# Performance work log

Hardware: AMD Instinct MI355X
Metric: run time of the kernel (lower is better)

Reference implementation:

```python
import jax, jax.numpy as jnp
import numpy as np

B, TE, TD, H = 4, 1024, 512, 128


def setup_inputs() -> dict:
    key = jax.random.key(0)
    k1, k2, k3, k4, k5 = jax.random.split(key, 5)
    return {
        "encoder_out": jax.random.normal(k1, (B, TE, H), dtype=jnp.float32),
        "decoder_out": jax.random.normal(k2, (B, TD, H), dtype=jnp.float32),
        "W_a": jax.random.normal(k3, (H, H), dtype=jnp.float32) * 0.05,
        "U_a": jax.random.normal(k4, (H, H), dtype=jnp.float32) * 0.05,
        "V_a": jax.random.normal(k5, (H, 1), dtype=jnp.float32) * 0.05,
    }


def reference(encoder_out, decoder_out, W_a, U_a, V_a):
    # Bahdanau additive attention, vectorized over all decoder steps at once.
    # (The original K.rnn loop has no true recurrence; steps are independent.)
    W_s = jnp.einsum('bth,hk->btk', encoder_out, W_a)   # [B, Te, H]
    U_h = jnp.einsum('bdh,hk->bdk', decoder_out, U_a)   # [B, Td, H]
    # energies: v^T tanh(W s_t + U h_d) -> [B, Td, Te]
    tanh_arg = jnp.tanh(W_s[:, None, :, :] + U_h[:, :, None, :])  # [B, Td, Te, H]
    e = jnp.einsum('bdth,ho->bdt', tanh_arg, V_a)
    e = jax.nn.softmax(e, axis=-1)                      # attention weights [B, Td, Te]
    # context vectors: weighted sum over encoder positions -> [B, Td, H]
    c = jnp.einsum('bdt,bth->bdh', e, encoder_out)
    return (c, e)
```

## Files before the change

kernel.cpp:

```cpp
#include <hip/hip_runtime.h>

#define BB    4
#define TE    1024
#define TD    512
#define HH    128
#define DTILE 4
#define TTILE 64
#define ESTR  (TE + 8)
#define LOG2E 1.4426950408889634f

typedef float f32x2 __attribute__((ext_vector_type(2)));

__device__ __forceinline__ f32x2 pk_fma(f32x2 a, f32x2 b, f32x2 c) {
    return __builtin_elementwise_fma(a, b, c);
}

__device__ __forceinline__ float tanh_eval(float x) {
    float e = __builtin_amdgcn_exp2f(2.0f * LOG2E * x);
    return 1.0f - 2.0f * __builtin_amdgcn_rcpf(e + 1.0f);
}

__global__ __launch_bounds__(512, 2) void proj_gemm(
    const float* __restrict__ enc, const float* __restrict__ dec,
    const float* __restrict__ Wa,  const float* __restrict__ Ua,
    float* __restrict__ out)
{
    __shared__ float Ws[HH * HH];
    __shared__ float Xs[16 * HH];

    const int tid = threadIdx.x;
    const int r0  = blockIdx.x * 16;

    const float* X; const float* W; int rX0;
    if (r0 < BB * TE) { X = enc; W = Wa; rX0 = r0; }
    else              { X = dec; W = Ua; rX0 = r0 - BB * TE; }

    #pragma unroll
    for (int i = 0; i < 8; ++i)
        *(float4*)&Ws[i * 2048 + tid * 4] =
            *(const float4*)&W[i * 2048 + tid * 4];

    {
        const int r = tid >> 5, c = tid & 31;
        *(float4*)&Xs[r * HH + c * 4] =
            *(const float4*)&X[(size_t)(rX0 + r) * HH + c * 4];
    }
    __syncthreads();

    const int rr = tid >> 5;
    const int c4 = tid & 31;

    f32x2 aL0 = {0.f, 0.f}, aH0 = {0.f, 0.f};
    f32x2 aL1 = {0.f, 0.f}, aH1 = {0.f, 0.f};

    const float* wc   = &Ws[c4 * 4];
    const float* xrow = &Xs[rr * HH];

    #pragma unroll 4
    for (int k = 0; k < HH; k += 4) {
        float4 w0 = *(const float4*)&wc[(k + 0) * HH];
        float4 w1 = *(const float4*)&wc[(k + 1) * HH];
        float4 w2 = *(const float4*)&wc[(k + 2) * HH];
        float4 w3 = *(const float4*)&wc[(k + 3) * HH];
        float4 xv = *(const float4*)&xrow[k];

        aL0 = pk_fma((f32x2){xv.x, xv.x}, (f32x2){w0.x, w0.y}, aL0);
        aH0 = pk_fma((f32x2){xv.x, xv.x}, (f32x2){w0.z, w0.w}, aH0);
        aL1 = pk_fma((f32x2){xv.y, xv.y}, (f32x2){w1.x, w1.y}, aL1);
        aH1 = pk_fma((f32x2){xv.y, xv.y}, (f32x2){w1.z, w1.w}, aH1);
        aL0 = pk_fma((f32x2){xv.z, xv.z}, (f32x2){w2.x, w2.y}, aL0);
        aH0 = pk_fma((f32x2){xv.z, xv.z}, (f32x2){w2.z, w2.w}, aH0);
        aL1 = pk_fma((f32x2){xv.w, xv.w}, (f32x2){w3.x, w3.y}, aL1);
        aH1 = pk_fma((f32x2){xv.w, xv.w}, (f32x2){w3.z, w3.w}, aH1);
    }

    f32x2 aL = aL0 + aL1;
    f32x2 aH = aH0 + aH1;

    float4 o;
    o.x = tanh_eval(aL.x); o.y = tanh_eval(aL.y);
    o.z = tanh_eval(aH.x); o.w = tanh_eval(aH.y);
    *(float4*)&out[(size_t)(r0 + rr) * HH + c4 * 4] = o;
}

__global__ __launch_bounds__(512, 4) void attn_fused(
    const float* __restrict__ enc,
    const float* __restrict__ ta,
    const float* __restrict__ tb,
    const float* __restrict__ Va,
    float* __restrict__ c_out,
    float* __restrict__ e_out)
{
    __shared__ float e_s[DTILE * ESTR];
    __shared__ float p_s[DTILE * TE];
    __shared__ float c_red[8 * DTILE * HH];

    const int tid = threadIdx.x;
    const int l   = tid & 63;
    const int w   = tid >> 6;
    const int b   = blockIdx.x >> 7;
    const int d0  = (blockIdx.x & 127) * DTILE;

    const int h4 = l & 31, tsub = l >> 5;
    const float* enc_w = enc + ((size_t)b * TE + w * 8) * HH;
    float4 X0[4], X1[4];
    #pragma unroll
    for (int k = 0; k < 4; ++k)
        X0[k] = *(const float4*)&enc_w[(size_t)(tsub * 4 + k) * HH + h4 * 4];

    {
        const int g  = l >> 3;
        const int hl = l & 7;
        const int dl = g & 3;
        const int rh = g >> 2;

        f32x2 Bl[4], Bh[4], Pl[4], Ph[4], Vl[4], Vh[4];
        #pragma unroll
        for (int j = 0; j < 4; ++j) {
            float4 vv = *(const float4*)&Va[(j * 8 + hl) * 4];
            float4 bb = *(const float4*)&tb[((size_t)b * TD + d0 + dl) * HH + (j * 8 + hl) * 4];
            Vl[j] = (f32x2){vv.x, vv.y};  Vh[j] = (f32x2){vv.z, vv.w};
            Bl[j] = (f32x2){bb.x, bb.y};  Bh[j] = (f32x2){bb.z, bb.w};
            Pl[j] = Vl[j] * Bl[j];        Ph[j] = Vh[j] * Bh[j];
        }

        const float* ta_b = ta + (size_t)b * TE * HH;

        auto rowOf = [&](int i) {
            return ((i >> 2) << 6) + w * 8 + ((i & 3) << 1) + rh;
        };

        float4 A0[4], A1[4];
        auto loadA = [&](int i, float4 (&A)[4]) {
            const float* base = ta_b + (size_t)rowOf(i) * HH;
            #pragma unroll
            for (int j = 0; j < 4; ++j)
                A[j] = *(const float4*)&base[(j * 8 + hl) * 4];
        };

        auto p1c = [&](int i, float4 (&A)[4]) {
            const f32x2 one2 = {1.0f, 1.0f};
            f32x2 n2[8], d2[8];
            #pragma unroll
            for (int j = 0; j < 4; ++j) {
                f32x2 Al = (f32x2){A[j].x, A[j].y};
                f32x2 Ah = (f32x2){A[j].z, A[j].w};
                n2[2 * j]     = pk_fma(Vl[j], Al, Pl[j]);
                n2[2 * j + 1] = pk_fma(Vh[j], Ah, Ph[j]);
                d2[2 * j]     = pk_fma(Al, Bl[j], one2);
                d2[2 * j + 1] = pk_fma(Ah, Bh[j], one2);
            }
            #pragma unroll
            for (int s = 4; s >= 1; s >>= 1) {
                #pragma unroll
                for (int k = 0; k < s; ++k) {
                    n2[k] = pk_fma(n2[2 * k], d2[2 * k + 1], n2[2 * k + 1] * d2[2 * k]);
                    d2[k] = d2[2 * k] * d2[2 * k + 1];
                }
            }
            float num = n2[0].x * d2[0].y + n2[0].y * d2[0].x;
            float den = d2[0].x * d2[0].y;
            float e = num * __builtin_amdgcn_rcpf(den);
            e += __shfl_xor(e, 1);
            e += __shfl_xor(e, 2);
            e += __shfl_xor(e, 4);
            if (hl == 0) e_s[dl * ESTR + rowOf(i)] = e;
        };

        loadA(0, A0);
        #pragma unroll 1
        for (int i = 0; i < 62; i += 2) {
            loadA(i + 1, A1);
            p1c(i, A0);
            loadA(i + 2, A0);
            p1c(i + 1, A1);
        }
        loadA(63, A1);
        p1c(62, A0);
        p1c(63, A1);
    }
    __syncthreads();

    {
        const int d2 = w & 3, hf = w >> 2;
        float ev[16];
        float m = -3.0e38f;
        #pragma unroll
        for (int i = 0; i < 16; ++i) {
            ev[i] = e_s[d2 * ESTR + i * 64 + l];
            m = fmaxf(m, ev[i]);
        }
        #pragma unroll
        for (int off = 32; off; off >>= 1) m = fmaxf(m, __shfl_xor(m, off));
        float s = 0.f;
        #pragma unroll
        for (int i = 0; i < 16; ++i) {
            ev[i] = __builtin_amdgcn_exp2f((ev[i] - m) * LOG2E);
            s += ev[i];
        }
        #pragma unroll
        for (int off = 32; off; off >>= 1) s += __shfl_xor(s, off);
        float inv = __builtin_amdgcn_rcpf(s);

        float* eo = e_out + ((size_t)b * TD + d0 + d2) * TE;
        #pragma unroll
        for (int i = 0; i < 8; ++i) {
            int ii = hf * 8 + i;
            float p = ev[ii] * inv;
            p_s[d2 * TE + ii * 64 + l] = p;
            eo[ii * 64 + l] = p;
        }
        __syncthreads();
    }

    f32x2 accL[DTILE], accH[DTILE];
    #pragma unroll
    for (int d = 0; d < DTILE; ++d) {
        accL[d] = (f32x2){0.f, 0.f};
        accH[d] = (f32x2){0.f, 0.f};
    }

    {
        auto loadX = [&](int tt, float4 (&X)[4]) {
            const float* base = enc_w + (size_t)tt * TTILE * HH;
            #pragma unroll
            for (int k = 0; k < 4; ++k)
                X[k] = *(const float4*)&base[(tsub * 4 + k) * HH + h4 * 4];
        };

        auto p3c = [&](int tt, float4 (&X)[4]) {
            float4 ep[DTILE];
            #pragma unroll
            for (int d = 0; d < DTILE; ++d)
                ep[d] = *(const float4*)&p_s[d * TE + tt * TTILE + w * 8 + tsub * 4];
            #pragma unroll
            for (int k = 0; k < 4; ++k) {
                f32x2 xL = (f32x2){X[k].x, X[k].y};
                f32x2 xH = (f32x2){X[k].z, X[k].w};
                #pragma unroll
                for (int d = 0; d < DTILE; ++d) {
                    float p = k == 0 ? ep[d].x : k == 1 ? ep[d].y
                            : k == 2 ? ep[d].z : ep[d].w;
                    f32x2 pv = (f32x2){p, p};
                    accL[d] = pk_fma(pv, xL, accL[d]);
                    accH[d] = pk_fma(pv, xH, accH[d]);
                }
            }
        };

        #pragma unroll 1
        for (int tt = 0; tt < 14; tt += 2) {
            loadX(tt + 1, X1);
            p3c(tt, X0);
            loadX(tt + 2, X0);
            p3c(tt + 1, X1);
        }
        loadX(15, X1);
        p3c(14, X0);
        p3c(15, X1);
    }

    float4 acc4[DTILE];
    #pragma unroll
    for (int d = 0; d < DTILE; ++d)
        acc4[d] = make_float4(accL[d].x, accL[d].y, accH[d].x, accH[d].y);
    #pragma unroll
    for (int d = 0; d < DTILE; ++d) {
        acc4[d].x += __shfl_xor(acc4[d].x, 32);
        acc4[d].y += __shfl_xor(acc4[d].y, 32);
        acc4[d].z += __shfl_xor(acc4[d].z, 32);
        acc4[d].w += __shfl_xor(acc4[d].w, 32);
    }
    if (tsub == 0) {
        #pragma unroll
        for (int d = 0; d < DTILE; ++d)
            *(float4*)&c_red[(w * DTILE + d) * HH + h4 * 4] = acc4[d];
    }
    __syncthreads();

    if (w < DTILE && l < 32) {
        float4 o = make_float4(0.f, 0.f, 0.f, 0.f);
        #pragma unroll
        for (int ww = 0; ww < 8; ++ww) {
            float4 p = *(const float4*)&c_red[(ww * DTILE + w) * HH + l * 4];
            o.x += p.x; o.y += p.y; o.z += p.z; o.w += p.w;
        }
        *(float4*)&c_out[((size_t)b * TD + d0 + w) * HH + l * 4] = o;
    }
}

extern "C" void kernel_launch(void* const* d_in, const int* in_sizes, int n_in,
                              void* d_out, int out_size, void* d_ws, size_t ws_size,
                              hipStream_t stream) {
    (void)in_sizes; (void)n_in; (void)out_size; (void)ws_size;

    const float* enc = (const float*)d_in[0];
    const float* dec = (const float*)d_in[1];
    const float* Wa  = (const float*)d_in[2];
    const float* Ua  = (const float*)d_in[3];
    const float* Va  = (const float*)d_in[4];

    float* c_out = (float*)d_out;
    float* e_out = (float*)d_out + BB * TD * HH;

    float* proj = (float*)d_ws;
    float* ta_p = proj;
    float* tb_p = proj + BB * TE * HH;

    proj_gemm<<<384, 512, 0, stream>>>(enc, dec, Wa, Ua, proj);
    attn_fused<<<(BB * TD) / DTILE, 512, 0, stream>>>(enc, ta_p, tb_p, Va, c_out, e_out);
}
```

Measured before the change: 121.4 us.

## Split fused attention kernel into separate energy/softmax and context kernels

Splits the single fused attention kernel into two launches. The first computes energies and softmax and writes the weights to the output. The second reloads those weights from global memory into shared memory and computes the context vectors. The aim is to cut shared-memory and register pressure per kernel so more blocks fit per CU, and to let each phase schedule independently. In exchange it adds a launch and a global round trip of the attention weights.

```diff
diff --git a/kernel.cpp b/kernel.cpp
--- a/kernel.cpp
+++ b/kernel.cpp
@@ -83,30 +83,19 @@
     *(float4*)&out[(size_t)(r0 + rr) * HH + c4 * 4] = o;
 }
 
-__global__ __launch_bounds__(512, 4) void attn_fused(
-    const float* __restrict__ enc,
+__global__ __launch_bounds__(512, 4) void attn_energy(
     const float* __restrict__ ta,
     const float* __restrict__ tb,
     const float* __restrict__ Va,
-    float* __restrict__ c_out,
     float* __restrict__ e_out)
 {
     __shared__ float e_s[DTILE * ESTR];
-    __shared__ float p_s[DTILE * TE];
-    __shared__ float c_red[8 * DTILE * HH];
 
     const int tid = threadIdx.x;
     const int l   = tid & 63;
     const int w   = tid >> 6;
     const int b   = blockIdx.x >> 7;
     const int d0  = (blockIdx.x & 127) * DTILE;
-
-    const int h4 = l & 31, tsub = l >> 5;
-    const float* enc_w = enc + ((size_t)b * TE + w * 8) * HH;
-    float4 X0[4], X1[4];
-    #pragma unroll
-    for (int k = 0; k < 4; ++k)
-        X0[k] = *(const float4*)&enc_w[(size_t)(tsub * 4 + k) * HH + h4 * 4];
 
     {
         const int g  = l >> 3;
@@ -206,12 +195,42 @@
         #pragma unroll
         for (int i = 0; i < 8; ++i) {
             int ii = hf * 8 + i;
-            float p = ev[ii] * inv;
-            p_s[d2 * TE + ii * 64 + l] = p;
-            eo[ii * 64 + l] = p;
-        }
-        __syncthreads();
-    }
+            eo[ii * 64 + l] = ev[ii] * inv;
+        }
+    }
+}
+
+__global__ __launch_bounds__(512, 4) void attn_ctx(
+    const float* __restrict__ enc,
+    const float* __restrict__ e_out,
+    float* __restrict__ c_out)
+{
+    __shared__ float p_s[DTILE * TE];
+    __shared__ float c_red[8 * DTILE * HH];
+
+    const int tid = threadIdx.x;
+    const int l   = tid & 63;
+    const int w   = tid >> 6;
+    const int b   = blockIdx.x >> 7;
+    const int d0  = (blockIdx.x & 127) * DTILE;
+
+    const int h4 = l & 31, tsub = l >> 5;
+    const float* enc_w = enc + ((size_t)b * TE + w * 8) * HH;
+
+    float4 X0[4], X1[4];
+    #pragma unroll
+    for (int k = 0; k < 4; ++k)
+        X0[k] = *(const float4*)&enc_w[(size_t)(tsub * 4 + k) * HH + h4 * 4];
+
+    {
+        const float* po = e_out + ((size_t)b * TD + d0) * TE;
+        #pragma unroll
+        for (int i = 0; i < 2; ++i) {
+            int idx = tid + i * 512;
+            *(float4*)&p_s[idx * 4] = *(const float4*)&po[idx * 4];
+        }
+    }
+    __syncthreads();
 
     f32x2 accL[DTILE], accH[DTILE];
     #pragma unroll
@@ -307,6 +326,7 @@
     float* ta_p = proj;
     float* tb_p = proj + BB * TE * HH;
 
-    proj_gemm<<<384, 512, 0, stream>>>(enc, dec, Wa, Ua, proj);
-    attn_fused<<<(BB * TD) / DTILE, 512, 0, stream>>>(enc, ta_p, tb_p, Va, c_out, e_out);
-}
+    proj_gemm<<<192 * 2, 512, 0, stream>>>(enc, dec, Wa, Ua, proj);
+    attn_energy<<<(BB * TD) / DTILE, 512, 0, stream>>>(ta_p, tb_p, Va, e_out);
+    attn_ctx<<<(BB * TD) / DTILE, 512, 0, stream>>>(enc, e_out, c_out);
+}
```

Result: no change. 123.8 us (+2.0%).
